# Kernel optimization log

Measured on AMD Instinct MI355X. Metric: run time of the kernel, lower is better.

Reference implementation:

```python
import jax, jax.numpy as jnp
import numpy as np

NUM_HEADS = 16

def setup_inputs() -> dict:
    key = jax.random.key(0)
    k1, k2, k3 = jax.random.split(key, 3)
    B, N, C = 2, 2048, 1024
    x = jax.random.normal(k1, (B, N, C), dtype=jnp.float32)
    w_qkv = jax.random.normal(k2, (C, 3 * C), dtype=jnp.float32) * (C ** -0.5)
    w_proj = jax.random.normal(k3, (C, C), dtype=jnp.float32) * (C ** -0.5)
    b_proj = jnp.zeros((C,), dtype=jnp.float32)
    return {"x": x, "w_qkv": w_qkv, "w_proj": w_proj, "b_proj": b_proj}

def reference(x, w_qkv, w_proj, b_proj):
    B, N, C = x.shape
    H = NUM_HEADS
    D = C // H
    scale = D ** -0.5
    qkv = (x @ w_qkv).reshape(B, N, 3, H, D).transpose(2, 0, 3, 1, 4)  # [3,B,H,N,D]
    q, k, v = qkv[0], qkv[1], qkv[2]
    attn = jnp.einsum("bhnd,bhmd->bhnm", q, k) * scale  # [B,H,N,N]
    attn = jax.nn.softmax(attn, axis=-1)
    out = jnp.einsum("bhnm,bhmd->bhnd", attn, v)  # [B,H,N,D]
    out = out.transpose(0, 2, 1, 3).reshape(B, N, C)
    return out @ w_proj + b_proj
```

## Files before the change

### kernel.cpp

```cpp
#include <hip/hip_runtime.h>
#include <hip/hip_bf16.h>
#include <math.h>

#define B_SZ   2
#define N_SEQ  2048
#define C_DIM  1024
#define H_NUM  16
#define D_HEAD 64
#define M_ROWS (B_SZ * N_SEQ)
#define QKV_N  (3 * C_DIM)

typedef __attribute__((ext_vector_type(8))) short  bf16x8;
typedef __attribute__((ext_vector_type(4))) float  floatx4;

static __device__ __forceinline__ unsigned short f2bf(float x) {
    unsigned int u = __float_as_uint(x);
    u = (u + 0x7FFFu + ((u >> 16) & 1u)) >> 16;
    return (unsigned short)u;
}
static __device__ __forceinline__ unsigned int f2bf_hi(float x) {
    unsigned int u = __float_as_uint(x);
    return u + 0x7FFFu + ((u >> 16) & 1u);
}

#if __has_builtin(__builtin_amdgcn_exp2f)
#define EXP2F(x) __builtin_amdgcn_exp2f(x)
#else
#define EXP2F(x) exp2f(x)
#endif

#define GLP(p) ((const __attribute__((address_space(1))) void*)(p))
#define LDP(p) ((__attribute__((address_space(3))) void*)(p))

__global__ __launch_bounds__(256)
void cvt_bf16(const float* __restrict__ in, unsigned short* __restrict__ out, int n4)
{
    const int i = blockIdx.x * 256 + threadIdx.x;
    if (i < n4) {
        float4 v = ((const float4*)in)[i];
        ushort4 p;
        p.x = f2bf(v.x); p.y = f2bf(v.y); p.z = f2bf(v.z); p.w = f2bf(v.w);
        ((ushort4*)out)[i] = p;
    }
}

__global__ __launch_bounds__(256)
void transpose_cvt(const float* __restrict__ W, unsigned short* __restrict__ WT,
                   int K, int N)
{
    __shared__ unsigned short t[64][72];
    const int tid = threadIdx.x;
    const int n0 = blockIdx.x * 64;
    const int k0 = blockIdx.y * 64;

    const int tc = tid & 15;
    const int tr = tid >> 4;
    #pragma unroll
    for (int p = 0; p < 4; ++p) {
        const int r = tr + p * 16;
        float4 v = *(const float4*)&W[(size_t)(k0 + r) * N + n0 + tc * 4];
        ushort4 pk;
        pk.x = f2bf(v.x); pk.y = f2bf(v.y); pk.z = f2bf(v.z); pk.w = f2bf(v.w);
        *(ushort4*)&t[r][tc * 4] = pk;
    }
    __syncthreads();

    const int n  = tid >> 2;
    const int c0 = (tid & 3) * 16;
    unsigned short tmp[16];
    #pragma unroll
    for (int i = 0; i < 16; ++i) tmp[i] = t[c0 + i][n];
    *(uint4*)&WT[(size_t)(n0 + n) * K + k0 + c0]     = *(uint4*)&tmp[0];
    *(uint4*)&WT[(size_t)(n0 + n) * K + k0 + c0 + 8] = *(uint4*)&tmp[8];
}

__global__ __launch_bounds__(256)
void gemm_qkv(const unsigned short* __restrict__ A,
              const unsigned short* __restrict__ BT,
              unsigned short* __restrict__ qbuf,
              unsigned short* __restrict__ kbuf,
              unsigned short* __restrict__ vbuf)
{
    const int K = C_DIM, N = QKV_N;
    __shared__ unsigned short As[128 * 32];
    __shared__ unsigned short Bs[128 * 32];

    const int tid  = threadIdx.x;
    const int lane = tid & 63;
    const int wave = tid >> 6;
    const int l15  = lane & 15;
    const int lq   = lane >> 4;
    const int wm   = (wave & 1) * 64;
    const int wn   = (wave >> 1) * 64;

    const int bm = blockIdx.y * 128;
    const int bn = blockIdx.x * 128;

    const int sr = tid >> 2;
    const int sc = (tid & 3) * 8;

    const unsigned short* ga0 = A  + (size_t)(bm + sr) * K + sc;
    const unsigned short* ga1 = A  + (size_t)(bm + 64 + sr) * K + sc;
    const unsigned short* gb0 = BT + (size_t)(bn + sr) * K + sc;
    const unsigned short* gb1 = BT + (size_t)(bn + 64 + sr) * K + sc;

    unsigned short* la0 = &As[sr * 32 + sc];
    unsigned short* la1 = &As[(64 + sr) * 32 + sc];
    unsigned short* lb0 = &Bs[sr * 32 + sc];
    unsigned short* lb1 = &Bs[(64 + sr) * 32 + sc];

    floatx4 acc[4][4];
    #pragma unroll
    for (int i = 0; i < 4; ++i)
        #pragma unroll
        for (int j = 0; j < 4; ++j) acc[i][j] = (floatx4){0.f, 0.f, 0.f, 0.f};

    for (int kt = 0; kt < K; kt += 32) {
        __builtin_amdgcn_global_load_lds(GLP(ga0), LDP(la0), 16, 0, 0);
        __builtin_amdgcn_global_load_lds(GLP(ga1), LDP(la1), 16, 0, 0);
        __builtin_amdgcn_global_load_lds(GLP(gb0), LDP(lb0), 16, 0, 0);
        __builtin_amdgcn_global_load_lds(GLP(gb1), LDP(lb1), 16, 0, 0);
        ga0 += 32; ga1 += 32; gb0 += 32; gb1 += 32;
        __syncthreads();

        bf16x8 af[4], bfr[4];
        #pragma unroll
        for (int t = 0; t < 4; ++t) {
            af[t]  = *(const bf16x8*)&As[(wm + t * 16 + l15) * 32 + lq * 8];
            bfr[t] = *(const bf16x8*)&Bs[(wn + t * 16 + l15) * 32 + lq * 8];
        }
        #pragma unroll
        for (int mt = 0; mt < 4; ++mt)
            #pragma unroll
            for (int nt = 0; nt < 4; ++nt)
                acc[mt][nt] = __builtin_amdgcn_mfma_f32_16x16x32_bf16(
                    af[mt], bfr[nt], acc[mt][nt], 0, 0, 0);
        __syncthreads();
    }

    #pragma unroll
    for (int nt = 0; nt < 4; ++nt) {
        const int col  = bn + wn + nt * 16 + l15;
        const int reg3 = col >> 10;
        const int h    = (col >> 6) & 15;
        const int d    = col & 63;
        #pragma unroll
        for (int mt = 0; mt < 4; ++mt) {
            const int row = bm + wm + mt * 16 + lq * 4;
            const int b   = row >> 11;
            const int n   = row & 2047;
            if (reg3 < 2) {
                unsigned short* dst = (reg3 ? kbuf : qbuf)
                    + ((size_t)(b * H_NUM + h) * N_SEQ + n) * D_HEAD + d;
                #pragma unroll
                for (int r = 0; r < 4; ++r)
                    dst[(size_t)r * D_HEAD] = f2bf(acc[mt][nt][r]);
            } else {
                const int a  = n & 63;
                const int fk = (a & 0x20) | ((a & 0x0C) << 1) | ((a & 0x10) >> 2);
                unsigned short* dst = vbuf
                    + ((size_t)(b * H_NUM + h) * D_HEAD + d) * N_SEQ + (n & ~63) + fk;
                ushort4 pk;
                pk.x = f2bf(acc[mt][nt][0]); pk.y = f2bf(acc[mt][nt][1]);
                pk.z = f2bf(acc[mt][nt][2]); pk.w = f2bf(acc[mt][nt][3]);
                *(ushort4*)dst = pk;
            }
        }
    }
}

__global__ __launch_bounds__(256)
void attn_mfma(const unsigned short* __restrict__ qbuf,
               const unsigned short* __restrict__ kbuf,
               const unsigned short* __restrict__ vbuf,
               unsigned short* __restrict__ attnb)
{
    __shared__ unsigned short KsS[2][64 * 64];
    __shared__ unsigned short VtS[2][64 * 64];

    const int tid  = threadIdx.x;
    const int lane = tid & 63;
    const int wave = tid >> 6;
    const int l15  = lane & 15;
    const int lq   = lane >> 4;
    const int e    = l15 & 7;

    const int bid  = blockIdx.x;
    const int bh   = (bid & 7) * 4 + (bid >> 8);
    const int qblk = (bid >> 3) & 31;
    const int b    = bh >> 4;
    const int h    = bh & 15;
    const int q0   = qblk * 64 + wave * 16;

    const unsigned short* khead = kbuf + (size_t)bh * N_SEQ * D_HEAD;
    const unsigned short* vhead = vbuf + (size_t)bh * D_HEAD * N_SEQ;
    const float cexp = 0.18033688011112042f;

    bf16x8 qf[2];
    {
        const unsigned short* qrow = qbuf
            + ((size_t)bh * N_SEQ + q0 + l15) * D_HEAD + lq * 8;
        qf[0] = *(const bf16x8*)qrow;
        qf[1] = *(const bf16x8*)(qrow + 32);
    }

    floatx4 acc[4];
    #pragma unroll
    for (int dc = 0; dc < 4; ++dc) acc[dc] = (floatx4){0.f, 0.f, 0.f, 0.f};
    float lsum = 0.f;

    const int srow = tid >> 3;
    const int gso  = ((tid & 7) ^ (srow & 7)) * 8;

    __builtin_amdgcn_global_load_lds(GLP(khead + (size_t)srow * 64 + gso),
                                     LDP(&KsS[0][tid * 8]), 16, 0, 0);
    __builtin_amdgcn_global_load_lds(GLP(khead + (size_t)(srow + 32) * 64 + gso),
                                     LDP(&KsS[0][2048 + tid * 8]), 16, 0, 0);
    __builtin_amdgcn_global_load_lds(GLP(vhead + (size_t)srow * N_SEQ + gso),
                                     LDP(&VtS[0][tid * 8]), 16, 0, 0);
    __builtin_amdgcn_global_load_lds(GLP(vhead + (size_t)(srow + 32) * N_SEQ + gso),
                                     LDP(&VtS[0][2048 + tid * 8]), 16, 0, 0);

    for (int tile = 0; tile < N_SEQ / 64; ++tile) {
        const int cur = tile & 1;
        __syncthreads();

        if (tile + 1 < N_SEQ / 64) {
            const int m1 = (tile + 1) * 64;
            const int nx = cur ^ 1;
            __builtin_amdgcn_global_load_lds(GLP(khead + (size_t)(m1 + srow) * 64 + gso),
                                             LDP(&KsS[nx][tid * 8]), 16, 0, 0);
            __builtin_amdgcn_global_load_lds(GLP(khead + (size_t)(m1 + srow + 32) * 64 + gso),
                                             LDP(&KsS[nx][2048 + tid * 8]), 16, 0, 0);
            __builtin_amdgcn_global_load_lds(GLP(vhead + (size_t)srow * N_SEQ + m1 + gso),
                                             LDP(&VtS[nx][tid * 8]), 16, 0, 0);
            __builtin_amdgcn_global_load_lds(GLP(vhead + (size_t)(srow + 32) * N_SEQ + m1 + gso),
                                             LDP(&VtS[nx][2048 + tid * 8]), 16, 0, 0);
        }

        const unsigned short* Ksc = &KsS[cur][0];
        const unsigned short* Vtc = &VtS[cur][0];

        floatx4 st[4];
        #pragma unroll
        for (int t = 0; t < 4; ++t) {
            bf16x8 k0 = *(const bf16x8*)&Ksc[(t * 16 + l15) * 64 + ((lq ^ e) * 8)];
            bf16x8 k1 = *(const bf16x8*)&Ksc[(t * 16 + l15) * 64 + (((4 + lq) ^ e) * 8)];
            floatx4 s = (floatx4){0.f, 0.f, 0.f, 0.f};
            s = __builtin_amdgcn_mfma_f32_16x16x32_bf16(k0, qf[0], s, 0, 0, 0);
            s = __builtin_amdgcn_mfma_f32_16x16x32_bf16(k1, qf[1], s, 0, 0, 0);
            st[t] = s;
        }

        unsigned int pk[8];
        float la = 0.f;
        #pragma unroll
        for (int t = 0; t < 4; ++t) {
            float p0 = EXP2F(fmaf(st[t][0], cexp, -8.f));
            float p1 = EXP2F(fmaf(st[t][1], cexp, -8.f));
            float p2 = EXP2F(fmaf(st[t][2], cexp, -8.f));
            float p3 = EXP2F(fmaf(st[t][3], cexp, -8.f));
            la += (p0 + p1) + (p2 + p3);
            pk[t * 2]     = __builtin_amdgcn_perm(f2bf_hi(p1), f2bf_hi(p0), 0x07060302u);
            pk[t * 2 + 1] = __builtin_amdgcn_perm(f2bf_hi(p3), f2bf_hi(p2), 0x07060302u);
        }
        lsum += la;
        union { uint4 u; bf16x8 v; } cvt0, cvt1;
        cvt0.u = make_uint4(pk[0], pk[1], pk[2], pk[3]);
        cvt1.u = make_uint4(pk[4], pk[5], pk[6], pk[7]);

        #pragma unroll
        for (int dc = 0; dc < 4; ++dc) {
            bf16x8 v0 = *(const bf16x8*)&Vtc[(dc * 16 + l15) * 64 + ((lq ^ e) * 8)];
            bf16x8 v1 = *(const bf16x8*)&Vtc[(dc * 16 + l15) * 64 + (((4 + lq) ^ e) * 8)];
            acc[dc] = __builtin_amdgcn_mfma_f32_16x16x32_bf16(v0, cvt0.v, acc[dc], 0, 0, 0);
            acc[dc] = __builtin_amdgcn_mfma_f32_16x16x32_bf16(v1, cvt1.v, acc[dc], 0, 0, 0);
        }
    }

    float l = lsum;
    l += __shfl_xor(l, 16, 64);
    l += __shfl_xor(l, 32, 64);
    const float inv = 1.f / l;
    const int q = q0 + l15;
    unsigned short* orow = attnb + ((size_t)b * N_SEQ + q) * C_DIM + h * D_HEAD;
    #pragma unroll
    for (int dc = 0; dc < 4; ++dc) {
        ushort4 pkk;
        pkk.x = f2bf(acc[dc][0] * inv);
        pkk.y = f2bf(acc[dc][1] * inv);
        pkk.z = f2bf(acc[dc][2] * inv);
        pkk.w = f2bf(acc[dc][3] * inv);
        *(ushort4*)&orow[dc * 16 + lq * 4] = pkk;
    }
}

__global__ __launch_bounds__(256)
void gemm_bt(const unsigned short* __restrict__ A,
             const unsigned short* __restrict__ BT,
             const float* __restrict__ bias,
             float* __restrict__ Cm,
             int M, int N, int K)
{
    __shared__ unsigned short As[128 * 32];
    __shared__ unsigned short Bs[64 * 32];

    const int tid  = threadIdx.x;
    const int lane = tid & 63;
    const int wave = tid >> 6;
    const int l15  = lane & 15;
    const int lq   = lane >> 4;
    const int wm   = (wave & 1) * 64;
    const int wn   = (wave >> 1) * 32;

    const int bm = blockIdx.y * 128;
    const int bn = blockIdx.x * 64;

    const int sr = tid >> 2;
    const int sc = (tid & 3) * 8;

    const unsigned short* ga0 = A  + (size_t)(bm + sr) * K + sc;
    const unsigned short* ga1 = A  + (size_t)(bm + 64 + sr) * K + sc;
    const unsigned short* gb0 = BT + (size_t)(bn + sr) * K + sc;

    unsigned short* la0 = &As[sr * 32 + sc];
    unsigned short* la1 = &As[(64 + sr) * 32 + sc];
    unsigned short* lb0 = &Bs[sr * 32 + sc];

    floatx4 acc[4][2];
    #pragma unroll
    for (int i = 0; i < 4; ++i)
        #pragma unroll
        for (int j = 0; j < 2; ++j) acc[i][j] = (floatx4){0.f, 0.f, 0.f, 0.f};

    for (int kt = 0; kt < K; kt += 32) {
        __builtin_amdgcn_global_load_lds(GLP(ga0), LDP(la0), 16, 0, 0);
        __builtin_amdgcn_global_load_lds(GLP(ga1), LDP(la1), 16, 0, 0);
        __builtin_amdgcn_global_load_lds(GLP(gb0), LDP(lb0), 16, 0, 0);
        ga0 += 32; ga1 += 32; gb0 += 32;
        __syncthreads();

        bf16x8 af[4], bfr[2];
        #pragma unroll
        for (int t = 0; t < 4; ++t)
            af[t] = *(const bf16x8*)&As[(wm + t * 16 + l15) * 32 + lq * 8];
        #pragma unroll
        for (int t = 0; t < 2; ++t)
            bfr[t] = *(const bf16x8*)&Bs[(wn + t * 16 + l15) * 32 + lq * 8];
        #pragma unroll
        for (int mt = 0; mt < 4; ++mt)
            #pragma unroll
            for (int nt = 0; nt < 2; ++nt)
                acc[mt][nt] = __builtin_amdgcn_mfma_f32_16x16x32_bf16(
                    af[mt], bfr[nt], acc[mt][nt], 0, 0, 0);
        __syncthreads();
    }

    float bv[2];
    #pragma unroll
    for (int nt = 0; nt < 2; ++nt) bv[nt] = bias[bn + wn + nt * 16 + l15];
    #pragma unroll
    for (int mt = 0; mt < 4; ++mt) {
        const int row = bm + wm + mt * 16 + lq * 4;
        #pragma unroll
        for (int nt = 0; nt < 2; ++nt) {
            const int col = bn + wn + nt * 16 + l15;
            #pragma unroll
            for (int r = 0; r < 4; ++r)
                Cm[(size_t)(row + r) * N + col] = acc[mt][nt][r] + bv[nt];
        }
    }
}

extern "C" void kernel_launch(void* const* d_in, const int* in_sizes, int n_in,
                              void* d_out, int out_size, void* d_ws, size_t ws_size,
                              hipStream_t stream)
{
    const float* x      = (const float*)d_in[0];
    const float* w_qkv  = (const float*)d_in[1];
    const float* w_proj = (const float*)d_in[2];
    const float* b_proj = (const float*)d_in[3];
    float*       out    = (float*)d_out;

    unsigned short* xb     = (unsigned short*)d_ws;
    unsigned short* wqkvT  = xb     + (size_t)M_ROWS * C_DIM;
    unsigned short* wprojT = wqkvT  + (size_t)QKV_N * C_DIM;
    unsigned short* qbuf   = wprojT + (size_t)C_DIM * C_DIM;
    unsigned short* kbuf   = qbuf   + (size_t)M_ROWS * C_DIM;
    unsigned short* vbuf   = kbuf   + (size_t)M_ROWS * C_DIM;
    unsigned short* attnb  = vbuf   + (size_t)M_ROWS * C_DIM;

    cvt_bf16<<<(M_ROWS * C_DIM / 4 + 255) / 256, 256, 0, stream>>>(x, xb, M_ROWS * C_DIM / 4);
    transpose_cvt<<<dim3(QKV_N / 64, C_DIM / 64), 256, 0, stream>>>(w_qkv, wqkvT, C_DIM, QKV_N);
    transpose_cvt<<<dim3(C_DIM / 64, C_DIM / 64), 256, 0, stream>>>(w_proj, wprojT, C_DIM, C_DIM);

    gemm_qkv<<<dim3(QKV_N / 128, M_ROWS / 128), 256, 0, stream>>>(xb, wqkvT, qbuf, kbuf, vbuf);

    attn_mfma<<<1024, 256, 0, stream>>>(qbuf, kbuf, vbuf, attnb);

    gemm_bt<<<dim3(C_DIM / 64, M_ROWS / 128), 256, 0, stream>>>(
        attnb, wprojT, b_proj, out, M_ROWS, C_DIM, C_DIM);
}
```

Measured before the change: 199.7 us.

## Fuse prep kernels, fold softmax scale into Q, vectorize Q/K stores

Merges the x conversion and both weight transpose-conversions into one launch to cut launch overhead. The QKV GEMM swaps MFMA operand order for Q/K tiles so each lane holds four consecutive head-dim values, which allows packed 8-byte stores instead of scattered 2-byte stores. The softmax exp2 scale is folded into Q at GEMM epilogue and the -8 offset into the MFMA accumulator init, removing an FMA per score in attention. Rounding Q after scaling slightly changes numerics.

Measured after the change: 208.9 us. 4.6% more time.

```diff
diff --git a/kernel.cpp b/kernel.cpp
--- a/kernel.cpp
+++ b/kernel.cpp
@@ -32,26 +32,35 @@
 #define GLP(p) ((const __attribute__((address_space(1))) void*)(p))
 #define LDP(p) ((__attribute__((address_space(3))) void*)(p))
 
+#define CEXP 0.18033688011112042f
+
 __global__ __launch_bounds__(256)
-void cvt_bf16(const float* __restrict__ in, unsigned short* __restrict__ out, int n4)
+void prep_fused(const float* __restrict__ x,      unsigned short* __restrict__ xb,
+                const float* __restrict__ w_qkv,  unsigned short* __restrict__ wqkvT,
+                const float* __restrict__ w_proj, unsigned short* __restrict__ wprojT)
 {
-    const int i = blockIdx.x * 256 + threadIdx.x;
-    if (i < n4) {
-        float4 v = ((const float4*)in)[i];
+    __shared__ unsigned short t[64][72];
+    const int bid = blockIdx.x;
+    const int tid = threadIdx.x;
+
+    if (bid < 4096) {
+        const int i = bid * 256 + tid;
+        float4 v = ((const float4*)x)[i];
         ushort4 p;
         p.x = f2bf(v.x); p.y = f2bf(v.y); p.z = f2bf(v.z); p.w = f2bf(v.w);
-        ((ushort4*)out)[i] = p;
-    }
-}
-
-__global__ __launch_bounds__(256)
-void transpose_cvt(const float* __restrict__ W, unsigned short* __restrict__ WT,
-                   int K, int N)
-{
-    __shared__ unsigned short t[64][72];
-    const int tid = threadIdx.x;
-    const int n0 = blockIdx.x * 64;
-    const int k0 = blockIdx.y * 64;
+        ((ushort4*)xb)[i] = p;
+        return;
+    }
+
+    const float* W;
+    unsigned short* WT;
+    int N, tt;
+    if (bid < 4096 + 768) { W = w_qkv;  WT = wqkvT;  N = QKV_N; tt = bid - 4096; }
+    else                  { W = w_proj; WT = wprojT; N = C_DIM; tt = bid - 4864; }
+    const int ntiles = N / 64;
+    const int n0 = (tt % ntiles) * 64;
+    const int k0 = (tt / ntiles) * 64;
+    const int K  = C_DIM;
 
     const int tc = tid & 15;
     const int tr = tid >> 4;
@@ -81,7 +90,7 @@
               unsigned short* __restrict__ kbuf,
               unsigned short* __restrict__ vbuf)
 {
-    const int K = C_DIM, N = QKV_N;
+    const int K = C_DIM;
     __shared__ unsigned short As[128 * 32];
     __shared__ unsigned short Bs[128 * 32];
 
@@ -95,6 +104,7 @@
 
     const int bm = blockIdx.y * 128;
     const int bn = blockIdx.x * 128;
+    const bool isv = (bn >= 2 * C_DIM);
 
     const int sr = tid >> 2;
     const int sc = (tid & 3) * 8;
@@ -129,41 +139,64 @@
             af[t]  = *(const bf16x8*)&As[(wm + t * 16 + l15) * 32 + lq * 8];
             bfr[t] = *(const bf16x8*)&Bs[(wn + t * 16 + l15) * 32 + lq * 8];
         }
-        #pragma unroll
-        for (int mt = 0; mt < 4; ++mt)
-            #pragma unroll
-            for (int nt = 0; nt < 4; ++nt)
-                acc[mt][nt] = __builtin_amdgcn_mfma_f32_16x16x32_bf16(
-                    af[mt], bfr[nt], acc[mt][nt], 0, 0, 0);
+        if (isv) {
+            #pragma unroll
+            for (int mt = 0; mt < 4; ++mt)
+                #pragma unroll
+                for (int nt = 0; nt < 4; ++nt)
+                    acc[mt][nt] = __builtin_amdgcn_mfma_f32_16x16x32_bf16(
+                        af[mt], bfr[nt], acc[mt][nt], 0, 0, 0);
+        } else {
+            #pragma unroll
+            for (int mt = 0; mt < 4; ++mt)
+                #pragma unroll
+                for (int nt = 0; nt < 4; ++nt)
+                    acc[mt][nt] = __builtin_amdgcn_mfma_f32_16x16x32_bf16(
+                        bfr[nt], af[mt], acc[mt][nt], 0, 0, 0);
+        }
         __syncthreads();
     }
 
-    #pragma unroll
-    for (int nt = 0; nt < 4; ++nt) {
-        const int col  = bn + wn + nt * 16 + l15;
-        const int reg3 = col >> 10;
-        const int h    = (col >> 6) & 15;
-        const int d    = col & 63;
-        #pragma unroll
-        for (int mt = 0; mt < 4; ++mt) {
-            const int row = bm + wm + mt * 16 + lq * 4;
-            const int b   = row >> 11;
-            const int n   = row & 2047;
-            if (reg3 < 2) {
-                unsigned short* dst = (reg3 ? kbuf : qbuf)
-                    + ((size_t)(b * H_NUM + h) * N_SEQ + n) * D_HEAD + d;
-                #pragma unroll
-                for (int r = 0; r < 4; ++r)
-                    dst[(size_t)r * D_HEAD] = f2bf(acc[mt][nt][r]);
-            } else {
-                const int a  = n & 63;
-                const int fk = (a & 0x20) | ((a & 0x0C) << 1) | ((a & 0x10) >> 2);
-                unsigned short* dst = vbuf
-                    + ((size_t)(b * H_NUM + h) * D_HEAD + d) * N_SEQ + (n & ~63) + fk;
+    if (!isv) {
+        const bool isq = (bn < C_DIM);
+        const float scq = isq ? CEXP : 1.0f;
+        unsigned short* dbuf = isq ? qbuf : kbuf;
+        #pragma unroll
+        for (int nt = 0; nt < 4; ++nt) {
+            const int colb = bn + wn + nt * 16 + lq * 4;
+            const int h    = (colb >> 6) & 15;
+            const int d    = colb & 63;
+            #pragma unroll
+            for (int mt = 0; mt < 4; ++mt) {
+                const int row = bm + wm + mt * 16 + l15;
+                const int b   = row >> 11;
+                const int n   = row & 2047;
+                ushort4 pk;
+                pk.x = f2bf(acc[mt][nt][0] * scq);
+                pk.y = f2bf(acc[mt][nt][1] * scq);
+                pk.z = f2bf(acc[mt][nt][2] * scq);
+                pk.w = f2bf(acc[mt][nt][3] * scq);
+                *(ushort4*)&dbuf[((size_t)(b * H_NUM + h) * N_SEQ + n) * D_HEAD + d] = pk;
+            }
+        }
+    } else {
+        #pragma unroll
+        for (int nt = 0; nt < 4; ++nt) {
+            const int col = bn + wn + nt * 16 + l15;
+            const int h   = (col >> 6) & 15;
+            const int d   = col & 63;
+            #pragma unroll
+            for (int mt = 0; mt < 4; ++mt) {
+                const int row = bm + wm + mt * 16 + lq * 4;
+                const int b   = row >> 11;
+                const int n   = row & 2047;
+                const int a   = n & 63;
+                const int fk  = (a & 0x20) | ((a & 0x0C) << 1) | ((a & 0x10) >> 2);
                 ushort4 pk;
                 pk.x = f2bf(acc[mt][nt][0]); pk.y = f2bf(acc[mt][nt][1]);
                 pk.z = f2bf(acc[mt][nt][2]); pk.w = f2bf(acc[mt][nt][3]);
-                *(ushort4*)dst = pk;
+                *(ushort4*)&vbuf[((size_t)(b * H_NUM + h) * D_HEAD + d) * N_SEQ
+                                 + (n & ~63) + fk] = pk;
             }
         }
     }
@@ -194,7 +227,6 @@
 
     const unsigned short* khead = kbuf + (size_t)bh * N_SEQ * D_HEAD;
     const unsigned short* vhead = vbuf + (size_t)bh * D_HEAD * N_SEQ;
-    const float cexp = 0.18033688011112042f;
 
     bf16x8 qf[2];
     {
@@ -246,7 +278,7 @@
         for (int t = 0; t < 4; ++t) {
             bf16x8 k0 = *(const bf16x8*)&Ksc[(t * 16 + l15) * 64 + ((lq ^ e) * 8)];
             bf16x8 k1 = *(const bf16x8*)&Ksc[(t * 16 + l15) * 64 + (((4 + lq) ^ e) * 8)];
-            floatx4 s = (floatx4){0.f, 0.f, 0.f, 0.f};
+            floatx4 s = (floatx4){-8.f, -8.f, -8.f, -8.f};
             s = __builtin_amdgcn_mfma_f32_16x16x32_bf16(k0, qf[0], s, 0, 0, 0);
             s = __builtin_amdgcn_mfma_f32_16x16x32_bf16(k1, qf[1], s, 0, 0, 0);
             st[t] = s;
@@ -256,10 +288,10 @@
         float la = 0.f;
         #pragma unroll
         for (int t = 0; t < 4; ++t) {
-            float p0 = EXP2F(fmaf(st[t][0], cexp, -8.f));
-            float p1 = EXP2F(fmaf(st[t][1], cexp, -8.f));
-            float p2 = EXP2F(fmaf(st[t][2], cexp, -8.f));
-            float p3 = EXP2F(fmaf(st[t][3], cexp, -8.f));
+            float p0 = EXP2F(st[t][0]);
+            float p1 = EXP2F(st[t][1]);
+            float p2 = EXP2F(st[t][2]);
+            float p3 = EXP2F(st[t][3]);
             la += (p0 + p1) + (p2 + p3);
             pk[t * 2]     = __builtin_amdgcn_perm(f2bf_hi(p1), f2bf_hi(p0), 0x07060302u);
             pk[t * 2 + 1] = __builtin_amdgcn_perm(f2bf_hi(p3), f2bf_hi(p2), 0x07060302u);
@@ -390,9 +422,7 @@
     unsigned short* vbuf   = kbuf   + (size_t)M_ROWS * C_DIM;
     unsigned short* attnb  = vbuf   + (size_t)M_ROWS * C_DIM;
 
-    cvt_bf16<<<(M_ROWS * C_DIM / 4 + 255) / 256, 256, 0, stream>>>(x, xb, M_ROWS * C_DIM / 4);
-    transpose_cvt<<<dim3(QKV_N / 64, C_DIM / 64), 256, 0, stream>>>(w_qkv, wqkvT, C_DIM, QKV_N);
-    transpose_cvt<<<dim3(C_DIM / 64, C_DIM / 64), 256, 0, stream>>>(w_proj, wprojT, C_DIM, C_DIM);
+    prep_fused<<<4096 + 768 + 256, 256, 0, stream>>>(x, xb, w_qkv, wqkvT, w_proj, wprojT);
 
     gemm_qkv<<<dim3(QKV_N / 128, M_ROWS / 128), 256, 0, stream>>>(xb, wqkvT, qbuf, kbuf, vbuf);
 
```
